# Kernel optimization log

Measured on AMD Instinct MI355X. Metric: run time of the kernel, lower is better.

The kernel has to match this reference:

```python
import jax, jax.numpy as jnp
import numpy as np

D_MODEL = 512
N_STATE = 64
EMB_DIM = 512
LN_EPS = 1e-5


def setup_inputs() -> dict:
    key = jax.random.key(0)
    ks = jax.random.split(key, 12)
    B, L, d, N, e = 8, 2048, D_MODEL, N_STATE, EMB_DIM
    x = jax.random.normal(ks[0], (B, L, d), dtype=jnp.float32)
    emb = jax.random.normal(ks[1], (B, e), dtype=jnp.float32)
    # S4D kernel params
    A_real = -0.5 * jnp.ones((d, N), dtype=jnp.float32)
    A_imag = jnp.pi * jnp.broadcast_to(jnp.arange(N, dtype=jnp.float32)[None, :], (d, N))
    C = jax.random.normal(ks[2], (d, N, 2), dtype=jnp.float32) * 0.5
    dt_min, dt_max = 0.001, 0.1
    log_dt = jax.random.uniform(ks[3], (d,), dtype=jnp.float32) * (np.log(dt_max) - np.log(dt_min)) + np.log(dt_min)
    B_ssm = jnp.ones((d, N), dtype=jnp.float32)  # buffer, treated as constant
    # block params
    D_skip = jax.random.normal(ks[4], (d,), dtype=jnp.float32) * 0.01
    ln_gamma = jnp.ones((d,), dtype=jnp.float32)
    ln_beta = jnp.zeros((d,), dtype=jnp.float32)
    lim_out = 1.0 / np.sqrt(d)
    W_out = jax.random.uniform(ks[5], (2 * d, d), dtype=jnp.float32, minval=-lim_out, maxval=lim_out)
    b_out = jax.random.uniform(ks[6], (2 * d,), dtype=jnp.float32, minval=-lim_out, maxval=lim_out)
    lim_f = 1.0 / np.sqrt(e)
    W_film = jax.random.uniform(ks[7], (2 * d, e), dtype=jnp.float32, minval=-lim_f, maxval=lim_f)
    b_film = jax.random.uniform(ks[8], (2 * d,), dtype=jnp.float32, minval=-lim_f, maxval=lim_f)
    return dict(x=x, emb=emb, A_real=A_real, A_imag=A_imag, C=C, log_dt=log_dt,
                B_ssm=B_ssm, D_skip=D_skip, ln_gamma=ln_gamma, ln_beta=ln_beta,
                W_out=W_out, b_out=b_out, W_film=W_film, b_film=b_film)


def reference(x, emb, A_real, A_imag, C, log_dt, B_ssm, D_skip, ln_gamma, ln_beta,
              W_out, b_out, W_film, b_film):
    Bsz, L, d = x.shape
    residual = x
    # LayerNorm
    mu = jnp.mean(x, axis=-1, keepdims=True)
    var = jnp.mean((x - mu) ** 2, axis=-1, keepdims=True)
    xn = (x - mu) * jax.lax.rsqrt(var + LN_EPS) * ln_gamma + ln_beta
    # S4D kernel: K[d,l] = Re( sum_n (C*B)[d,n] * exp(dt*A)[d,n]**l ) * dt[d]
    dt = jnp.exp(log_dt)                                 # (d,)
    A = A_real + 1j * A_imag                             # (d,N)
    dtA = A * dt[:, None]                                # (d,N)
    Cc = (C[..., 0] + 1j * C[..., 1]) * B_ssm            # (d,N) complex
    l = jnp.arange(L, dtype=jnp.float32)
    powers = jnp.exp(dtA[:, :, None] * l)                # (d,N,L) complex, A_bar**l
    K = jnp.einsum('dn,dnl->dl', Cc, powers).real * dt[:, None]  # (d,L)
    # FFT convolution (circular over 2L -> linear)
    x_t = jnp.transpose(xn, (0, 2, 1))                   # (B,d,L)
    K_f = jnp.fft.rfft(K, n=2 * L)                       # (d,L+1)
    x_f = jnp.fft.rfft(x_t, n=2 * L)                     # (B,d,L+1)
    y = jnp.fft.irfft(K_f[None] * x_f, n=2 * L)[..., :L] # (B,d,L)
    y = y + x_t * D_skip[None, :, None]
    y = jnp.transpose(y, (0, 2, 1))                      # (B,L,d)
    # FiLM conditioning
    film = jax.nn.silu(emb) @ W_film.T + b_film          # (B,2d)
    scale, shift = jnp.split(film, 2, axis=-1)
    y = y * (1.0 + scale[:, None, :]) + shift[:, None, :]
    # out_proj: Linear(d,2d) + GLU
    proj = y @ W_out.T + b_out                           # (B,L,2d)
    a, g = jnp.split(proj, 2, axis=-1)
    y = a * jax.nn.sigmoid(g)
    return residual + y
```

## Files before the change

kernel.cpp:

```cpp
#include <hip/hip_runtime.h>
#include <math.h>

typedef __attribute__((ext_vector_type(8))) short bf8v;
typedef __attribute__((ext_vector_type(4))) float f4v;

union BF8 { bf8v v; unsigned short e[8]; };

__device__ __forceinline__ float bf2f(unsigned short u) {
  union { unsigned int i; float f; } c; c.i = ((unsigned int)u) << 16; return c.f;
}
__device__ __forceinline__ unsigned short f2bf(float f) {
  union { float f; unsigned int i; } c; c.f = f;
  return (unsigned short)((c.i + 0x7fffu + ((c.i >> 16) & 1u)) >> 16);
}
__device__ __forceinline__ void gld16(const unsigned short* g, unsigned short* l) {
  __builtin_amdgcn_global_load_lds(
      (const __attribute__((address_space(1))) unsigned int*)g,
      (__attribute__((address_space(3))) unsigned int*)l, 16, 0, 0);
}

__global__ __launch_bounds__(64) void ln_kernel(const float* __restrict__ x,
    const float* __restrict__ gamma, const float* __restrict__ beta,
    unsigned short* __restrict__ xn) {
  const int row = blockIdx.x;
  const int lane = threadIdx.x;
  const float4* xr = (const float4*)(x + (size_t)row * 512);
  const float4 v0 = xr[lane * 2], v1 = xr[lane * 2 + 1];
  float s  = v0.x + v0.y + v0.z + v0.w + v1.x + v1.y + v1.z + v1.w;
  float sq = v0.x*v0.x + v0.y*v0.y + v0.z*v0.z + v0.w*v0.w
           + v1.x*v1.x + v1.y*v1.y + v1.z*v1.z + v1.w*v1.w;
  #pragma unroll
  for (int off = 32; off >= 1; off >>= 1) {
    s  += __shfl_xor(s, off);
    sq += __shfl_xor(sq, off);
  }
  const float mu   = s * (1.f / 512.f);
  const float var  = sq * (1.f / 512.f) - mu * mu;
  const float rstd = rsqrtf(var + 1e-5f);
  const float4* gp = (const float4*)gamma + lane * 2;
  const float4* bp = (const float4*)beta  + lane * 2;
  const float4 g0 = gp[0], g1 = gp[1], bb0 = bp[0], bb1 = bp[1];
  const float o0 = (v0.x - mu) * rstd * g0.x + bb0.x;
  const float o1 = (v0.y - mu) * rstd * g0.y + bb0.y;
  const float o2 = (v0.z - mu) * rstd * g0.z + bb0.z;
  const float o3 = (v0.w - mu) * rstd * g0.w + bb0.w;
  const float o4 = (v1.x - mu) * rstd * g1.x + bb1.x;
  const float o5 = (v1.y - mu) * rstd * g1.y + bb1.y;
  const float o6 = (v1.z - mu) * rstd * g1.z + bb1.z;
  const float o7 = (v1.w - mu) * rstd * g1.w + bb1.w;
  uint4 pk;
  pk.x = (unsigned)f2bf(o0) | ((unsigned)f2bf(o1) << 16);
  pk.y = (unsigned)f2bf(o2) | ((unsigned)f2bf(o3) << 16);
  pk.z = (unsigned)f2bf(o4) | ((unsigned)f2bf(o5) << 16);
  pk.w = (unsigned)f2bf(o6) | ((unsigned)f2bf(o7) << 16);
  ((uint4*)(xn + (size_t)row * 512))[lane] = pk;
}

__global__ __launch_bounds__(256) void film_kernel(const float* __restrict__ emb,
    const float* __restrict__ Wf, const float* __restrict__ bfm,
    float* __restrict__ film) {
  const int gw = blockIdx.x * 4 + (threadIdx.x >> 6);
  const int lane = threadIdx.x & 63;
  const int b = gw >> 10, j = gw & 1023;
  const float4* ep = (const float4*)(emb + (size_t)b * 512) + lane * 2;
  const float4* wp = (const float4*)(Wf + (size_t)j * 512) + lane * 2;
  float acc = 0.f;
  #pragma unroll
  for (int i = 0; i < 2; i++) {
    const float4 e = ep[i], w = wp[i];
    acc += (e.x / (1.f + __expf(-e.x))) * w.x;
    acc += (e.y / (1.f + __expf(-e.y))) * w.y;
    acc += (e.z / (1.f + __expf(-e.z))) * w.z;
    acc += (e.w / (1.f + __expf(-e.w))) * w.w;
  }
  #pragma unroll
  for (int off = 32; off >= 1; off >>= 1) acc += __shfl_xor(acc, off);
  if (lane == 0) film[(size_t)b * 1024 + j] = acc + bfm[j];
}

__global__ __launch_bounds__(256) void wcvt_kernel(const float* __restrict__ W,
    unsigned short* __restrict__ Wb) {
  const int i = blockIdx.x * 256 + threadIdx.x;
  const float4 v = ((const float4*)W)[i];
  uint2 pk;
  pk.x = (unsigned)f2bf(v.x) | ((unsigned)f2bf(v.y) << 16);
  pk.y = (unsigned)f2bf(v.z) | ((unsigned)f2bf(v.w) << 16);
  ((uint2*)Wb)[i] = pk;
}

__global__ __launch_bounds__(256) void tr_kernel(const unsigned short* __restrict__ in,
    unsigned short* __restrict__ out, int R, int C) {
  __shared__ __align__(16) unsigned short t[64 * 72];
  const int c0 = blockIdx.x * 64, r0 = blockIdx.y * 64;
  const int tid = threadIdx.x;
  #pragma unroll
  for (int i = 0; i < 2; i++) {
    const int idx = tid + i * 256;
    const int r = idx >> 3, q = idx & 7;
    const uint4 v = *(const uint4*)(in + (size_t)(r0 + r) * C + c0 + q * 8);
    *(uint4*)&t[r * 72 + ((q ^ (r >> 3)) * 8)] = v;
  }
  __syncthreads();
  #pragma unroll
  for (int i = 0; i < 2; i++) {
    const int idx = tid + i * 256;
    const int c = idx >> 3, g = idx & 7;
    union { unsigned short s[8]; uint4 u; } pk;
    #pragma unroll
    for (int j = 0; j < 8; j++)
      pk.s[j] = t[(g * 8 + j) * 72 + (((c >> 3) ^ g) * 8) + (c & 7)];
    *(uint4*)(out + (size_t)(c0 + c) * R + r0 + g * 8) = pk.u;
  }
}

__global__ __launch_bounds__(256) void ktab_kernel(const float* __restrict__ A_real,
    const float* __restrict__ A_imag, const float* __restrict__ Cc,
    const float* __restrict__ log_dt, const float* __restrict__ B_ssm,
    const float* __restrict__ D_skip, float* __restrict__ Kt) {
  const int d = blockIdx.x * 4 + (threadIdx.x >> 6);
  const int n = threadIdx.x & 63;
  const int dn = d * 64 + n;
  const float dt = __expf(log_dt[d]);
  const float er = __expf(dt * A_real[dn]);
  float sw, cw; __sincosf(dt * A_imag[dn], &sw, &cw);
  const float wre = er * cw, wim = er * sw;
  const float bs = B_ssm[dn] * dt;
  float pre = Cc[dn * 2] * bs, pim = Cc[dn * 2 + 1] * bs;
  const float dsk = D_skip[d];
  for (int tau = 0; tau < 64; tau++) {
    float r = pre;
    #pragma unroll
    for (int off = 32; off >= 1; off >>= 1) r += __shfl_xor(r, off);
    if (n == 0) Kt[d * 64 + tau] = (tau == 0) ? (r + dsk) : r;
    const float nre = pre * wre - pim * wim;
    const float nim = pre * wim + pim * wre;
    pre = nre; pim = nim;
  }
}

__global__ __launch_bounds__(256) void tab_kernel(
    const float* __restrict__ A_real, const float* __restrict__ A_imag,
    const float* __restrict__ Cc, const float* __restrict__ log_dt,
    const float* __restrict__ B_ssm, const float* __restrict__ Kt,
    unsigned short* __restrict__ Pre, unsigned short* __restrict__ Pim,
    unsigned short* __restrict__ Mre, unsigned short* __restrict__ Mim,
    unsigned short* __restrict__ Tt, float* __restrict__ W64r, float* __restrict__ W64i) {
  const int d = blockIdx.x;
  const int tid = threadIdx.x;
  const float dt = __expf(log_dt[d]);
  for (int g = tid; g < 512; g += 256) {
    const int n = g >> 3, s0 = (g & 7) * 8;
    const int dn = d * 64 + n;
    const float ar = dt * A_real[dn], ai = dt * A_imag[dn];
    union { unsigned short s[8]; uint4 u; } pr, pi;
    #pragma unroll
    for (int j = 0; j < 8; j++) {
      const float k = (float)(63 - (s0 + j));
      const float ex = __expf(ar * k);
      float sn, cs; __sincosf(ai * k, &sn, &cs);
      pr.s[j] = f2bf(ex * cs); pi.s[j] = f2bf(ex * sn);
    }
    *(uint4*)(Pre + (size_t)d * 4096 + n * 64 + s0) = pr.u;
    *(uint4*)(Pim + (size_t)d * 4096 + n * 64 + s0) = pi.u;
  }
  for (int g = tid; g < 512; g += 256) {
    const int t = g >> 3, n0 = (g & 7) * 8;
    union { unsigned short s[8]; uint4 u; } mr, mi;
    #pragma unroll
    for (int j = 0; j < 8; j++) {
      const int dn = d * 64 + n0 + j;
      const float ar = dt * A_real[dn], ai = dt * A_imag[dn];
      const float bs = B_ssm[dn] * dt;
      const float c0 = Cc[dn * 2] * bs, c1 = Cc[dn * 2 + 1] * bs;
      const float k = (float)(t + 1);
      const float ex = __expf(ar * k);
      float sn, cs; __sincosf(ai * k, &sn, &cs);
      mr.s[j] = f2bf(ex * (c0 * cs - c1 * sn));
      mi.s[j] = f2bf(-ex * (c0 * sn + c1 * cs));
    }
    *(uint4*)(Mre + (size_t)d * 4096 + t * 64 + n0) = mr.u;
    *(uint4*)(Mim + (size_t)d * 4096 + t * 64 + n0) = mi.u;
  }
  for (int g = tid; g < 512; g += 256) {
    const int t = g >> 3, s0 = (g & 7) * 8;
    union { unsigned short s[8]; uint4 u; } tv;
    #pragma unroll
    for (int j = 0; j < 8; j++) {
      const int s = s0 + j;
      tv.s[j] = (s <= t) ? f2bf(Kt[d * 64 + (t - s)]) : (unsigned short)0;
    }
    *(uint4*)(Tt + (size_t)d * 4096 + t * 64 + s0) = tv.u;
  }
  if (tid < 64) {
    const int dn = d * 64 + tid;
    const float ex = __expf(dt * A_real[dn] * 64.f);
    float sn, cs; __sincosf(dt * A_imag[dn] * 64.f, &sn, &cs);
    W64r[d * 64 + tid] = ex * cs;
    W64i[d * 64 + tid] = ex * sn;
  }
}

__global__ __launch_bounds__(256, 2) void ssm_kernel(
    const unsigned short* __restrict__ xT,
    const unsigned short* __restrict__ Pre, const unsigned short* __restrict__ Pim,
    const unsigned short* __restrict__ Mre, const unsigned short* __restrict__ Mim,
    const unsigned short* __restrict__ Tt,
    const float* __restrict__ W64r, const float* __restrict__ W64i,
    const float* __restrict__ film, unsigned short* __restrict__ y2) {
  extern __shared__ char smem[];
  unsigned int*   Eb  = (unsigned int*)smem;
  unsigned short* Ibr = (unsigned short*)(smem + 64 * 133 * 4);
  unsigned short* Ibi = Ibr + 128 * 72;

  const int bx = blockIdx.x;
  const int d = bx & 511, h = bx >> 9;
  const int tid = threadIdx.x;
  const int wv = tid >> 6, lane = tid & 63;
  const int n15 = lane & 15, quad = lane >> 4;
  const int j0 = wv * 32;
  const int jg0 = h * 128;
  const size_t dtab = (size_t)d * 4096;

  bf8v Xf[2][2];
  #pragma unroll
  for (int ct = 0; ct < 2; ct++)
    #pragma unroll
    for (int kq = 0; kq < 2; kq++) {
      const int j = j0 + ct * 16 + n15;
      Xf[ct][kq] = *(const bf8v*)(xT + (size_t)d * 16384 + (jg0 + j) * 64 + kq * 32 + quad * 8);
    }

  {
    f4v Er[4][2], Ei[4][2];
    #pragma unroll
    for (int a = 0; a < 4; a++)
      #pragma unroll
      for (int b2 = 0; b2 < 2; b2++) { Er[a][b2] = (f4v){0,0,0,0}; Ei[a][b2] = (f4v){0,0,0,0}; }
    #pragma unroll
    for (int mt = 0; mt < 4; mt++)
      #pragma unroll
      for (int kq = 0; kq < 2; kq++) {
        const bf8v pr = *(const bf8v*)(Pre + dtab + (mt * 16 + n15) * 64 + kq * 32 + quad * 8);
        const bf8v pi = *(const bf8v*)(Pim + dtab + (mt * 16 + n15) * 64 + kq * 32 + quad * 8);
        #pragma unroll
        for (int ct = 0; ct < 2; ct++) {
          Er[mt][ct] = __builtin_amdgcn_mfma_f32_16x16x32_bf16(pr, Xf[ct][kq], Er[mt][ct], 0, 0, 0);
          Ei[mt][ct] = __builtin_amdgcn_mfma_f32_16x16x32_bf16(pi, Xf[ct][kq], Ei[mt][ct], 0, 0, 0);
        }
      }
    #pragma unroll
    for (int mt = 0; mt < 4; mt++)
      #pragma unroll
      for (int ct = 0; ct < 2; ct++)
        #pragma unroll
        for (int i = 0; i < 4; i++) {
          const int row = mt * 16 + quad * 4 + i;
          const int col = j0 + ct * 16 + n15;
          Eb[row * 133 + col] =
              (unsigned)f2bf(Er[mt][ct][i]) | ((unsigned)f2bf(Ei[mt][ct][i]) << 16);
        }
  }
  __syncthreads();

  {
    const int n = tid & 63, bp = tid >> 6;
    const float wre = W64r[d * 64 + n], wim = W64i[d * 64 + n];
    unsigned int eb[32];
    #pragma unroll
    for (int c = 0; c < 32; c++) eb[c] = Eb[n * 133 + bp * 32 + c];
    float str = 0.f, sti = 0.f;
    #pragma unroll
    for (int c = 0; c < 32; c++) {
      const int j = bp * 32 + c;
      Ibr[j * 72 + n] = f2bf(str);
      Ibi[j * 72 + n] = f2bf(sti);
      const float er = bf2f((unsigned short)(eb[c] & 0xffffu));
      const float ei = bf2f((unsigned short)(eb[c] >> 16));
      const float nr = er + wre * str - wim * sti;
      const float ni = ei + wre * sti + wim * str;
      str = nr; sti = ni;
    }
  }
  __syncthreads();

  f4v Y[4][2];
  #pragma unroll
  for (int a = 0; a < 4; a++)
    #pragma unroll
    for (int b2 = 0; b2 < 2; b2++) Y[a][b2] = (f4v){0,0,0,0};

  #pragma unroll
  for (int mt = 0; mt < 4; mt++)
    #pragma unroll
    for (int kq = 0; kq < 2; kq++) {
      const bf8v tf = *(const bf8v*)(Tt + dtab + (mt * 16 + n15) * 64 + kq * 32 + quad * 8);
      #pragma unroll
      for (int ct = 0; ct < 2; ct++)
        Y[mt][ct] = __builtin_amdgcn_mfma_f32_16x16x32_bf16(tf, Xf[ct][kq], Y[mt][ct], 0, 0, 0);
    }

  #pragma unroll
  for (int kq = 0; kq < 2; kq++) {
    bf8v irf[2], iif[2];
    #pragma unroll
    for (int ct = 0; ct < 2; ct++) {
      const int j = j0 + ct * 16 + n15;
      irf[ct] = *(const bf8v*)&Ibr[j * 72 + kq * 32 + quad * 8];
      iif[ct] = *(const bf8v*)&Ibi[j * 72 + kq * 32 + quad * 8];
    }
    #pragma unroll
    for (int mt = 0; mt < 4; mt++) {
      const bf8v mr = *(const bf8v*)(Mre + dtab + (mt * 16 + n15) * 64 + kq * 32 + quad * 8);
      const bf8v mi = *(const bf8v*)(Mim + dtab + (mt * 16 + n15) * 64 + kq * 32 + quad * 8);
      #pragma unroll
      for (int ct = 0; ct < 2; ct++) {
        Y[mt][ct] = __builtin_amdgcn_mfma_f32_16x16x32_bf16(mr, irf[ct], Y[mt][ct], 0, 0, 0);
        Y[mt][ct] = __builtin_amdgcn_mfma_f32_16x16x32_bf16(mi, iif[ct], Y[mt][ct], 0, 0, 0);
      }
    }
  }

  #pragma unroll
  for (int ct = 0; ct < 2; ct++) {
    const int jl = j0 + ct * 16 + n15;
    const int jglob = jg0 + jl;
    const int b = jglob >> 5;
    const float scl = 1.f + film[b * 1024 + d];
    const float shf = film[b * 1024 + 512 + d];
    #pragma unroll
    for (int mt = 0; mt < 4; mt++) {
      union { unsigned short s[4]; uint2 u; } pk;
      #pragma unroll
      for (int i = 0; i < 4; i++)
        pk.s[i] = f2bf(fmaf(Y[mt][ct][i], scl, shf));
      *(uint2*)(y2 + (size_t)d * 16384 + jglob * 64 + mt * 16 + quad * 4) = pk.u;
    }
  }
}

__global__ __launch_bounds__(256, 3) void gemm_kernel(
    const unsigned short* __restrict__ y2n, const unsigned short* __restrict__ Wb,
    const float* __restrict__ bo, const float* __restrict__ x,
    float* __restrict__ out) {
  __shared__ __align__(16) unsigned short Al[128 * 32];
  __shared__ __align__(16) unsigned short Bl[128 * 32];
  const int m0 = blockIdx.x * 128, ct = blockIdx.y;
  const int tid = threadIdx.x;
  const int wv = tid >> 6, lane = tid & 63;
  const int n15 = lane & 15, quad = lane >> 4;
  const int srow = lane >> 2;
  const int sk = (lane & 3) * 8;

  f4v acc[2][8];
  #pragma unroll
  for (int mi = 0; mi < 2; mi++)
    #pragma unroll
    for (int t4 = 0; t4 < 8; t4++) acc[mi][t4] = (f4v){0.f, 0.f, 0.f, 0.f};

  for (int kk = 0; kk < 16; kk++) {
    #pragma unroll
    for (int i = 0; i < 2; i++) {
      const int row = wv * 32 + i * 16 + srow;
      gld16(y2n + (size_t)(m0 + row) * 512 + kk * 32 + sk, Al + wv * 1024 + i * 512);
      const int c = (row < 64) ? (ct * 64 + row) : (512 + ct * 64 + (row - 64));
      gld16(Wb + (size_t)c * 512 + kk * 32 + sk, Bl + wv * 1024 + i * 512);
    }
    __syncthreads();
    bf8v a0 = *(const bf8v*)&Al[(wv * 32 + n15) * 32 + quad * 8];
    bf8v a1 = *(const bf8v*)&Al[(wv * 32 + 16 + n15) * 32 + quad * 8];
    #pragma unroll
    for (int t4 = 0; t4 < 8; t4++) {
      const bf8v bb = *(const bf8v*)&Bl[(t4 * 16 + n15) * 32 + quad * 8];
      acc[0][t4] = __builtin_amdgcn_mfma_f32_16x16x32_bf16(a0, bb, acc[0][t4], 0, 0, 0);
      acc[1][t4] = __builtin_amdgcn_mfma_f32_16x16x32_bf16(a1, bb, acc[1][t4], 0, 0, 0);
    }
    __syncthreads();
  }
  #pragma unroll
  for (int mi = 0; mi < 2; mi++) {
    const int mrow = m0 + wv * 32 + mi * 16 + quad * 4;
    #pragma unroll
    for (int t4 = 0; t4 < 4; t4++) {
      const int c = ct * 64 + t4 * 16 + n15;
      const float ba = bo[c], bg = bo[512 + c];
      #pragma unroll
      for (int i = 0; i < 4; i++) {
        const size_t off = (size_t)(mrow + i) * 512 + c;
        const float av = acc[mi][t4][i] + ba;
        const float gv = acc[mi][t4 + 4][i] + bg;
        out[off] = x[off] + av * (1.f / (1.f + __expf(-gv)));
      }
    }
  }
}

extern "C" void kernel_launch(void* const* d_in, const int* in_sizes, int n_in,
                              void* d_out, int out_size, void* d_ws, size_t ws_size,
                              hipStream_t stream) {
  const float* x      = (const float*)d_in[0];
  const float* emb    = (const float*)d_in[1];
  const float* A_real = (const float*)d_in[2];
  const float* A_imag = (const float*)d_in[3];
  const float* C      = (const float*)d_in[4];
  const float* log_dt = (const float*)d_in[5];
  const float* B_ssm  = (const float*)d_in[6];
  const float* D_skip = (const float*)d_in[7];
  const float* gamma  = (const float*)d_in[8];
  const float* beta   = (const float*)d_in[9];
  const float* W_out  = (const float*)d_in[10];
  const float* b_out  = (const float*)d_in[11];
  const float* W_film = (const float*)d_in[12];
  const float* b_film = (const float*)d_in[13];
  float* out = (float*)d_out;

  char* ws = (char*)d_ws;
  size_t o = 0;
  float*          film = (float*)(ws + o);          o += 32768;
  unsigned short* xn   = (unsigned short*)(ws + o); o += 16777216;
  unsigned short* xT   = (unsigned short*)(ws + o); o += 16777216;
  float*          Kt   = (float*)(ws + o);          o += 131072;
  unsigned short* Wb   = (unsigned short*)(ws + o); o += 1048576;
  unsigned short* Pre  = (unsigned short*)(ws + o); o += 4194304;
  unsigned short* Pim  = (unsigned short*)(ws + o); o += 4194304;
  unsigned short* Mre  = (unsigned short*)(ws + o); o += 4194304;
  unsigned short* Mim  = (unsigned short*)(ws + o); o += 4194304;
  unsigned short* Tt   = (unsigned short*)(ws + o); o += 4194304;
  float*          W64r = (float*)(ws + o);          o += 131072;
  float*          W64i = (float*)(ws + o);          o += 131072;
  unsigned short* y2   = xn;
  unsigned short* y2n  = xT;

  film_kernel<<<dim3(2048), dim3(256), 0, stream>>>(emb, W_film, b_film, film);
  ln_kernel<<<dim3(16384), dim3(64), 0, stream>>>(x, gamma, beta, xn);
  wcvt_kernel<<<dim3(512), dim3(256), 0, stream>>>(W_out, Wb);
  ktab_kernel<<<dim3(128), dim3(256), 0, stream>>>(A_real, A_imag, C, log_dt, B_ssm, D_skip, Kt);
  tab_kernel<<<dim3(512), dim3(256), 0, stream>>>(A_real, A_imag, C, log_dt, B_ssm, Kt,
                                                  Pre, Pim, Mre, Mim, Tt, W64r, W64i);
  tr_kernel<<<dim3(8, 256), dim3(256), 0, stream>>>(xn, xT, 16384, 512);
  ssm_kernel<<<dim3(1024), dim3(256), 70912, stream>>>(xT, Pre, Pim, Mre, Mim, Tt,
                                                       W64r, W64i, film, y2);
  tr_kernel<<<dim3(256, 8), dim3(256), 0, stream>>>(y2, y2n, 512, 16384);
  gemm_kernel<<<dim3(128, 8), dim3(256), 0, stream>>>(y2n, Wb, b_out, x, out);
}
```

Baseline: 205.3 us.

## Fuse prelude kernels, fuse LayerNorm with transpose, shrink SSM tiles, widen GEMM K-step

Film, weight conversion, kernel-tap and table generation are merged into one prelude launch, and the K taps are now computed directly in shared memory instead of through a global buffer. LayerNorm now writes its transposed output directly, which removes one transpose pass and the intermediate buffer. The SSM kernel uses half-size blocks with static shared memory and targets higher occupancy. The GEMM uses a 64-wide K step with XOR-swizzled LDS. The gain comes from fewer launches and less memory traffic, at the cost of more blocks and a different load balance.

```diff
diff --git a/kernel.cpp b/kernel.cpp
--- a/kernel.cpp
+++ b/kernel.cpp
@@ -19,73 +19,173 @@
       (__attribute__((address_space(3))) unsigned int*)l, 16, 0, 0);
 }
 
-__global__ __launch_bounds__(64) void ln_kernel(const float* __restrict__ x,
+__global__ __launch_bounds__(256) void prelude_kernel(
+    const float* __restrict__ emb, const float* __restrict__ Wf,
+    const float* __restrict__ bfm, float* __restrict__ film,
+    const float* __restrict__ W, unsigned short* __restrict__ Wb,
+    const float* __restrict__ A_real, const float* __restrict__ A_imag,
+    const float* __restrict__ Cc, const float* __restrict__ log_dt,
+    const float* __restrict__ B_ssm, const float* __restrict__ D_skip,
+    unsigned short* __restrict__ Pre, unsigned short* __restrict__ Pim,
+    unsigned short* __restrict__ Mre, unsigned short* __restrict__ Mim,
+    unsigned short* __restrict__ Tt, float* __restrict__ W64r, float* __restrict__ W64i) {
+  __shared__ float Ktl[64];
+  const int blk = blockIdx.x;
+  const int tid = threadIdx.x;
+  if (blk < 2048) {
+    const int gw = blk * 4 + (tid >> 6);
+    const int lane = tid & 63;
+    const int b = gw >> 10, j = gw & 1023;
+    const float4* ep = (const float4*)(emb + (size_t)b * 512) + lane * 2;
+    const float4* wp = (const float4*)(Wf + (size_t)j * 512) + lane * 2;
+    float acc = 0.f;
+    #pragma unroll
+    for (int i = 0; i < 2; i++) {
+      const float4 e = ep[i], w = wp[i];
+      acc += (e.x / (1.f + __expf(-e.x))) * w.x;
+      acc += (e.y / (1.f + __expf(-e.y))) * w.y;
+      acc += (e.z / (1.f + __expf(-e.z))) * w.z;
+      acc += (e.w / (1.f + __expf(-e.w))) * w.w;
+    }
+    #pragma unroll
+    for (int off = 32; off >= 1; off >>= 1) acc += __shfl_xor(acc, off);
+    if (lane == 0) film[(size_t)b * 1024 + j] = acc + bfm[j];
+  } else if (blk < 2560) {
+    const int i = (blk - 2048) * 256 + tid;
+    const float4 v = ((const float4*)W)[i];
+    uint2 pk;
+    pk.x = (unsigned)f2bf(v.x) | ((unsigned)f2bf(v.y) << 16);
+    pk.y = (unsigned)f2bf(v.z) | ((unsigned)f2bf(v.w) << 16);
+    ((uint2*)Wb)[i] = pk;
+  } else {
+    const int d = blk - 2560;
+    const float dt = __expf(log_dt[d]);
+    const int wv = tid >> 6, n = tid & 63;
+    {
+      const int dn = d * 64 + n;
+      const float ar = dt * A_real[dn], ai = dt * A_imag[dn];
+      const float bs = B_ssm[dn] * dt;
+      const float c0 = Cc[dn * 2] * bs, c1 = Cc[dn * 2 + 1] * bs;
+      #pragma unroll
+      for (int i = 0; i < 16; i++) {
+        const float tau = (float)(wv * 16 + i);
+        const float ex = __expf(ar * tau);
+        float sn, cs; __sincosf(ai * tau, &sn, &cs);
+        float r = ex * (c0 * cs - c1 * sn);
+        #pragma unroll
+        for (int off = 32; off >= 1; off >>= 1) r += __shfl_xor(r, off);
+        if (n == 0) Ktl[wv * 16 + i] = (wv * 16 + i == 0) ? (r + D_skip[d]) : r;
+      }
+    }
+    __syncthreads();
+    for (int g = tid; g < 512; g += 256) {
+      const int nn = g >> 3, s0 = (g & 7) * 8;
+      const int dn = d * 64 + nn;
+      const float ar = dt * A_real[dn], ai = dt * A_imag[dn];
+      union { unsigned short s[8]; uint4 u; } pr, pi;
+      #pragma unroll
+      for (int j = 0; j < 8; j++) {
+        const float k = (float)(63 - (s0 + j));
+        const float ex = __expf(ar * k);
+        float sn, cs; __sincosf(ai * k, &sn, &cs);
+        pr.s[j] = f2bf(ex * cs); pi.s[j] = f2bf(ex * sn);
+      }
+      *(uint4*)(Pre + (size_t)d * 4096 + nn * 64 + s0) = pr.u;
+      *(uint4*)(Pim + (size_t)d * 4096 + nn * 64 + s0) = pi.u;
+    }
+    for (int g = tid; g < 512; g += 256) {
+      const int t = g >> 3, n0 = (g & 7) * 8;
+      union { unsigned short s[8]; uint4 u; } mr, mi;
+      #pragma unroll
+      for (int j = 0; j < 8; j++) {
+        const int dn = d * 64 + n0 + j;
+        const float ar = dt * A_real[dn], ai = dt * A_imag[dn];
+        const float bs = B_ssm[dn] * dt;
+        const float c0 = Cc[dn * 2] * bs, c1 = Cc[dn * 2 + 1] * bs;
+        const float k = (float)(t + 1);
+        const float ex = __expf(ar * k);
+        float sn, cs; __sincosf(ai * k, &sn, &cs);
+        mr.s[j] = f2bf(ex * (c0 * cs - c1 * sn));
+        mi.s[j] = f2bf(-ex * (c0 * sn + c1 * cs));
+      }
+      *(uint4*)(Mre + (size_t)d * 4096 + t * 64 + n0) = mr.u;
+      *(uint4*)(Mim + (size_t)d * 4096 + t * 64 + n0) = mi.u;
+    }
+    for (int g = tid; g < 512; g += 256) {
+      const int t = g >> 3, s0 = (g & 7) * 8;
+      union { unsigned short s[8]; uint4 u; } tv;
+      #pragma unroll
+      for (int j = 0; j < 8; j++) {
+        const int s = s0 + j;
+        tv.s[j] = (s <= t) ? f2bf(Ktl[t - s]) : (unsigned short)0;
+      }
+      *(uint4*)(Tt + (size_t)d * 4096 + t * 64 + s0) = tv.u;
+    }
+    if (tid < 64) {
+      const int dn = d * 64 + tid;
+      const float ex = __expf(dt * A_real[dn] * 64.f);
+      float sn, cs; __sincosf(dt * A_imag[dn] * 64.f, &sn, &cs);
+      W64r[d * 64 + tid] = ex * cs;
+      W64i[d * 64 + tid] = ex * sn;
+    }
+  }
+}
+
+__global__ __launch_bounds__(256) void lnt_kernel(const float* __restrict__ x,
     const float* __restrict__ gamma, const float* __restrict__ beta,
-    unsigned short* __restrict__ xn) {
-  const int row = blockIdx.x;
-  const int lane = threadIdx.x;
-  const float4* xr = (const float4*)(x + (size_t)row * 512);
-  const float4 v0 = xr[lane * 2], v1 = xr[lane * 2 + 1];
-  float s  = v0.x + v0.y + v0.z + v0.w + v1.x + v1.y + v1.z + v1.w;
-  float sq = v0.x*v0.x + v0.y*v0.y + v0.z*v0.z + v0.w*v0.w
-           + v1.x*v1.x + v1.y*v1.y + v1.z*v1.z + v1.w*v1.w;
-  #pragma unroll
-  for (int off = 32; off >= 1; off >>= 1) {
-    s  += __shfl_xor(s, off);
-    sq += __shfl_xor(sq, off);
-  }
-  const float mu   = s * (1.f / 512.f);
-  const float var  = sq * (1.f / 512.f) - mu * mu;
-  const float rstd = rsqrtf(var + 1e-5f);
+    unsigned short* __restrict__ xT) {
+  __shared__ __align__(16) unsigned short t[16 * 520];
+  const int r0 = blockIdx.x * 16;
+  const int tid = threadIdx.x, wv = tid >> 6, lane = tid & 63;
   const float4* gp = (const float4*)gamma + lane * 2;
   const float4* bp = (const float4*)beta  + lane * 2;
   const float4 g0 = gp[0], g1 = gp[1], bb0 = bp[0], bb1 = bp[1];
-  const float o0 = (v0.x - mu) * rstd * g0.x + bb0.x;
-  const float o1 = (v0.y - mu) * rstd * g0.y + bb0.y;
-  const float o2 = (v0.z - mu) * rstd * g0.z + bb0.z;
-  const float o3 = (v0.w - mu) * rstd * g0.w + bb0.w;
-  const float o4 = (v1.x - mu) * rstd * g1.x + bb1.x;
-  const float o5 = (v1.y - mu) * rstd * g1.y + bb1.y;
-  const float o6 = (v1.z - mu) * rstd * g1.z + bb1.z;
-  const float o7 = (v1.w - mu) * rstd * g1.w + bb1.w;
-  uint4 pk;
-  pk.x = (unsigned)f2bf(o0) | ((unsigned)f2bf(o1) << 16);
-  pk.y = (unsigned)f2bf(o2) | ((unsigned)f2bf(o3) << 16);
-  pk.z = (unsigned)f2bf(o4) | ((unsigned)f2bf(o5) << 16);
-  pk.w = (unsigned)f2bf(o6) | ((unsigned)f2bf(o7) << 16);
-  ((uint4*)(xn + (size_t)row * 512))[lane] = pk;
-}
-
-__global__ __launch_bounds__(256) void film_kernel(const float* __restrict__ emb,
-    const float* __restrict__ Wf, const float* __restrict__ bfm,
-    float* __restrict__ film) {
-  const int gw = blockIdx.x * 4 + (threadIdx.x >> 6);
-  const int lane = threadIdx.x & 63;
-  const int b = gw >> 10, j = gw & 1023;
-  const float4* ep = (const float4*)(emb + (size_t)b * 512) + lane * 2;
-  const float4* wp = (const float4*)(Wf + (size_t)j * 512) + lane * 2;
-  float acc = 0.f;
-  #pragma unroll
-  for (int i = 0; i < 2; i++) {
-    const float4 e = ep[i], w = wp[i];
-    acc += (e.x / (1.f + __expf(-e.x))) * w.x;
-    acc += (e.y / (1.f + __expf(-e.y))) * w.y;
-    acc += (e.z / (1.f + __expf(-e.z))) * w.z;
-    acc += (e.w / (1.f + __expf(-e.w))) * w.w;
-  }
-  #pragma unroll
-  for (int off = 32; off >= 1; off >>= 1) acc += __shfl_xor(acc, off);
-  if (lane == 0) film[(size_t)b * 1024 + j] = acc + bfm[j];
-}
-
-__global__ __launch_bounds__(256) void wcvt_kernel(const float* __restrict__ W,
-    unsigned short* __restrict__ Wb) {
-  const int i = blockIdx.x * 256 + threadIdx.x;
-  const float4 v = ((const float4*)W)[i];
-  uint2 pk;
-  pk.x = (unsigned)f2bf(v.x) | ((unsigned)f2bf(v.y) << 16);
-  pk.y = (unsigned)f2bf(v.z) | ((unsigned)f2bf(v.w) << 16);
-  ((uint2*)Wb)[i] = pk;
+  #pragma unroll
+  for (int i = 0; i < 4; i++) {
+    const int r = wv * 4 + i;
+    const float4* xr = (const float4*)(x + (size_t)(r0 + r) * 512) + lane * 2;
+    const float4 v0 = xr[0], v1 = xr[1];
+    float s  = v0.x + v0.y + v0.z + v0.w + v1.x + v1.y + v1.z + v1.w;
+    float sq = v0.x*v0.x + v0.y*v0.y + v0.z*v0.z + v0.w*v0.w
+             + v1.x*v1.x + v1.y*v1.y + v1.z*v1.z + v1.w*v1.w;
+    #pragma unroll
+    for (int off = 32; off >= 1; off >>= 1) {
+      s  += __shfl_xor(s, off);
+      sq += __shfl_xor(sq, off);
+    }
+    const float mu   = s * (1.f / 512.f);
+    const float var  = sq * (1.f / 512.f) - mu * mu;
+    const float rstd = rsqrtf(var + 1e-5f);
+    uint4 pk;
+    pk.x = (unsigned)f2bf((v0.x - mu) * rstd * g0.x + bb0.x)
+         | ((unsigned)f2bf((v0.y - mu) * rstd * g0.y + bb0.y) << 16);
+    pk.y = (unsigned)f2bf((v0.z - mu) * rstd * g0.z + bb0.z)
+         | ((unsigned)f2bf((v0.w - mu) * rstd * g0.w + bb0.w) << 16);
+    pk.z = (unsigned)f2bf((v1.x - mu) * rstd * g1.x + bb1.x)
+         | ((unsigned)f2bf((v1.y - mu) * rstd * g1.y + bb1.y) << 16);
+    pk.w = (unsigned)f2bf((v1.z - mu) * rstd * g1.z + bb1.z)
+         | ((unsigned)f2bf((v1.w - mu) * rstd * g1.w + bb1.w) << 16);
+    *(uint4*)&t[r * 520 + lane * 8] = pk;
+  }
+  __syncthreads();
+  const int p = tid;
+  union { unsigned short s[8]; uint4 u; } a0, a1, b0, b1;
+  #pragma unroll
+  for (int r = 0; r < 8; r++) {
+    const unsigned v = *(const unsigned*)&t[r * 520 + p * 2];
+    a0.s[r] = (unsigned short)(v & 0xffffu);
+    b0.s[r] = (unsigned short)(v >> 16);
+  }
+  #pragma unroll
+  for (int r = 0; r < 8; r++) {
+    const unsigned v = *(const unsigned*)&t[(r + 8) * 520 + p * 2];
+    a1.s[r] = (unsigned short)(v & 0xffffu);
+    b1.s[r] = (unsigned short)(v >> 16);
+  }
+  unsigned short* o0 = xT + (size_t)(2 * p) * 16384 + r0;
+  *(uint4*)o0 = a0.u; *(uint4*)(o0 + 8) = a1.u;
+  unsigned short* o1 = xT + (size_t)(2 * p + 1) * 16384 + r0;
+  *(uint4*)o1 = b0.u; *(uint4*)(o1 + 8) = b1.u;
 }
 
 __global__ __launch_bounds__(256) void tr_kernel(const unsigned short* __restrict__ in,
@@ -113,217 +213,104 @@
   }
 }
 
-__global__ __launch_bounds__(256) void ktab_kernel(const float* __restrict__ A_real,
-    const float* __restrict__ A_imag, const float* __restrict__ Cc,
-    const float* __restrict__ log_dt, const float* __restrict__ B_ssm,
-    const float* __restrict__ D_skip, float* __restrict__ Kt) {
-  const int d = blockIdx.x * 4 + (threadIdx.x >> 6);
-  const int n = threadIdx.x & 63;
-  const int dn = d * 64 + n;
-  const float dt = __expf(log_dt[d]);
-  const float er = __expf(dt * A_real[dn]);
-  float sw, cw; __sincosf(dt * A_imag[dn], &sw, &cw);
-  const float wre = er * cw, wim = er * sw;
-  const float bs = B_ssm[dn] * dt;
-  float pre = Cc[dn * 2] * bs, pim = Cc[dn * 2 + 1] * bs;
-  const float dsk = D_skip[d];
-  for (int tau = 0; tau < 64; tau++) {
-    float r = pre;
-    #pragma unroll
-    for (int off = 32; off >= 1; off >>= 1) r += __shfl_xor(r, off);
-    if (n == 0) Kt[d * 64 + tau] = (tau == 0) ? (r + dsk) : r;
-    const float nre = pre * wre - pim * wim;
-    const float nim = pre * wim + pim * wre;
-    pre = nre; pim = nim;
-  }
-}
-
-__global__ __launch_bounds__(256) void tab_kernel(
-    const float* __restrict__ A_real, const float* __restrict__ A_imag,
-    const float* __restrict__ Cc, const float* __restrict__ log_dt,
-    const float* __restrict__ B_ssm, const float* __restrict__ Kt,
-    unsigned short* __restrict__ Pre, unsigned short* __restrict__ Pim,
-    unsigned short* __restrict__ Mre, unsigned short* __restrict__ Mim,
-    unsigned short* __restrict__ Tt, float* __restrict__ W64r, float* __restrict__ W64i) {
-  const int d = blockIdx.x;
-  const int tid = threadIdx.x;
-  const float dt = __expf(log_dt[d]);
-  for (int g = tid; g < 512; g += 256) {
-    const int n = g >> 3, s0 = (g & 7) * 8;
-    const int dn = d * 64 + n;
-    const float ar = dt * A_real[dn], ai = dt * A_imag[dn];
-    union { unsigned short s[8]; uint4 u; } pr, pi;
-    #pragma unroll
-    for (int j = 0; j < 8; j++) {
-      const float k = (float)(63 - (s0 + j));
-      const float ex = __expf(ar * k);
-      float sn, cs; __sincosf(ai * k, &sn, &cs);
-      pr.s[j] = f2bf(ex * cs); pi.s[j] = f2bf(ex * sn);
-    }
-    *(uint4*)(Pre + (size_t)d * 4096 + n * 64 + s0) = pr.u;
-    *(uint4*)(Pim + (size_t)d * 4096 + n * 64 + s0) = pi.u;
-  }
-  for (int g = tid; g < 512; g += 256) {
-    const int t = g >> 3, n0 = (g & 7) * 8;
-    union { unsigned short s[8]; uint4 u; } mr, mi;
-    #pragma unroll
-    for (int j = 0; j < 8; j++) {
-      const int dn = d * 64 + n0 + j;
-      const float ar = dt * A_real[dn], ai = dt * A_imag[dn];
-      const float bs = B_ssm[dn] * dt;
-      const float c0 = Cc[dn * 2] * bs, c1 = Cc[dn * 2 + 1] * bs;
-      const float k = (float)(t + 1);
-      const float ex = __expf(ar * k);
-      float sn, cs; __sincosf(ai * k, &sn, &cs);
-      mr.s[j] = f2bf(ex * (c0 * cs - c1 * sn));
-      mi.s[j] = f2bf(-ex * (c0 * sn + c1 * cs));
-    }
-    *(uint4*)(Mre + (size_t)d * 4096 + t * 64 + n0) = mr.u;
-    *(uint4*)(Mim + (size_t)d * 4096 + t * 64 + n0) = mi.u;
-  }
-  for (int g = tid; g < 512; g += 256) {
-    const int t = g >> 3, s0 = (g & 7) * 8;
-    union { unsigned short s[8]; uint4 u; } tv;
-    #pragma unroll
-    for (int j = 0; j < 8; j++) {
-      const int s = s0 + j;
-      tv.s[j] = (s <= t) ? f2bf(Kt[d * 64 + (t - s)]) : (unsigned short)0;
-    }
-    *(uint4*)(Tt + (size_t)d * 4096 + t * 64 + s0) = tv.u;
-  }
-  if (tid < 64) {
-    const int dn = d * 64 + tid;
-    const float ex = __expf(dt * A_real[dn] * 64.f);
-    float sn, cs; __sincosf(dt * A_imag[dn] * 64.f, &sn, &cs);
-    W64r[d * 64 + tid] = ex * cs;
-    W64i[d * 64 + tid] = ex * sn;
-  }
-}
-
-__global__ __launch_bounds__(256, 2) void ssm_kernel(
+__global__ __launch_bounds__(256, 4) void ssm_kernel(
     const unsigned short* __restrict__ xT,
     const unsigned short* __restrict__ Pre, const unsigned short* __restrict__ Pim,
     const unsigned short* __restrict__ Mre, const unsigned short* __restrict__ Mim,
     const unsigned short* __restrict__ Tt,
     const float* __restrict__ W64r, const float* __restrict__ W64i,
     const float* __restrict__ film, unsigned short* __restrict__ y2) {
-  extern __shared__ char smem[];
-  unsigned int*   Eb  = (unsigned int*)smem;
-  unsigned short* Ibr = (unsigned short*)(smem + 64 * 133 * 4);
-  unsigned short* Ibi = Ibr + 128 * 72;
+  __shared__ unsigned int Eb[64 * 66];
+  __shared__ unsigned short Ibr[64 * 72], Ibi[64 * 72];
 
   const int bx = blockIdx.x;
   const int d = bx & 511, h = bx >> 9;
   const int tid = threadIdx.x;
   const int wv = tid >> 6, lane = tid & 63;
   const int n15 = lane & 15, quad = lane >> 4;
-  const int j0 = wv * 32;
-  const int jg0 = h * 128;
+  const int j0 = wv * 16;
+  const int jg0 = h * 64;
   const size_t dtab = (size_t)d * 4096;
 
-  bf8v Xf[2][2];
-  #pragma unroll
-  for (int ct = 0; ct < 2; ct++)
-    #pragma unroll
-    for (int kq = 0; kq < 2; kq++) {
-      const int j = j0 + ct * 16 + n15;
-      Xf[ct][kq] = *(const bf8v*)(xT + (size_t)d * 16384 + (jg0 + j) * 64 + kq * 32 + quad * 8);
-    }
+  bf8v Xf[2];
+  #pragma unroll
+  for (int kq = 0; kq < 2; kq++)
+    Xf[kq] = *(const bf8v*)(xT + (size_t)d * 16384 + (jg0 + j0 + n15) * 64 + kq * 32 + quad * 8);
 
   {
-    f4v Er[4][2], Ei[4][2];
-    #pragma unroll
-    for (int a = 0; a < 4; a++)
-      #pragma unroll
-      for (int b2 = 0; b2 < 2; b2++) { Er[a][b2] = (f4v){0,0,0,0}; Ei[a][b2] = (f4v){0,0,0,0}; }
+    f4v Er[4], Ei[4];
+    #pragma unroll
+    for (int a = 0; a < 4; a++) { Er[a] = (f4v){0,0,0,0}; Ei[a] = (f4v){0,0,0,0}; }
     #pragma unroll
     for (int mt = 0; mt < 4; mt++)
       #pragma unroll
       for (int kq = 0; kq < 2; kq++) {
         const bf8v pr = *(const bf8v*)(Pre + dtab + (mt * 16 + n15) * 64 + kq * 32 + quad * 8);
         const bf8v pi = *(const bf8v*)(Pim + dtab + (mt * 16 + n15) * 64 + kq * 32 + quad * 8);
-        #pragma unroll
-        for (int ct = 0; ct < 2; ct++) {
-          Er[mt][ct] = __builtin_amdgcn_mfma_f32_16x16x32_bf16(pr, Xf[ct][kq], Er[mt][ct], 0, 0, 0);
-          Ei[mt][ct] = __builtin_amdgcn_mfma_f32_16x16x32_bf16(pi, Xf[ct][kq], Ei[mt][ct], 0, 0, 0);
-        }
+        Er[mt] = __builtin_amdgcn_mfma_f32_16x16x32_bf16(pr, Xf[kq], Er[mt], 0, 0, 0);
+        Ei[mt] = __builtin_amdgcn_mfma_f32_16x16x32_bf16(pi, Xf[kq], Ei[mt], 0, 0, 0);
       }
     #pragma unroll
     for (int mt = 0; mt < 4; mt++)
       #pragma unroll
-      for (int ct = 0; ct < 2; ct++)
-        #pragma unroll
-        for (int i = 0; i < 4; i++) {
-          const int row = mt * 16 + quad * 4 + i;
-          const int col = j0 + ct * 16 + n15;
-          Eb[row * 133 + col] =
-              (unsigned)f2bf(Er[mt][ct][i]) | ((unsigned)f2bf(Ei[mt][ct][i]) << 16);
-        }
+      for (int i = 0; i < 4; i++) {
+        const int row = mt * 16 + quad * 4 + i;
+        Eb[row * 66 + j0 + n15] =
+            (unsigned)f2bf(Er[mt][i]) | ((unsigned)f2bf(Ei[mt][i]) << 16);
+      }
   }
   __syncthreads();
 
   {
     const int n = tid & 63, bp = tid >> 6;
-    const float wre = W64r[d * 64 + n], wim = W64i[d * 64 + n];
-    unsigned int eb[32];
-    #pragma unroll
-    for (int c = 0; c < 32; c++) eb[c] = Eb[n * 133 + bp * 32 + c];
-    float str = 0.f, sti = 0.f;
-    #pragma unroll
-    for (int c = 0; c < 32; c++) {
-      const int j = bp * 32 + c;
-      Ibr[j * 72 + n] = f2bf(str);
-      Ibi[j * 72 + n] = f2bf(sti);
-      const float er = bf2f((unsigned short)(eb[c] & 0xffffu));
-      const float ei = bf2f((unsigned short)(eb[c] >> 16));
-      const float nr = er + wre * str - wim * sti;
-      const float ni = ei + wre * sti + wim * str;
-      str = nr; sti = ni;
+    if (bp < 2) {
+      const float wre = W64r[d * 64 + n], wim = W64i[d * 64 + n];
+      unsigned int eb[32];
+      #pragma unroll
+      for (int c = 0; c < 32; c++) eb[c] = Eb[n * 66 + bp * 32 + c];
+      float str = 0.f, sti = 0.f;
+      #pragma unroll
+      for (int c = 0; c < 32; c++) {
+        const int j = bp * 32 + c;
+        Ibr[j * 72 + n] = f2bf(str);
+        Ibi[j * 72 + n] = f2bf(sti);
+        const float er = bf2f((unsigned short)(eb[c] & 0xffffu));
+        const float ei = bf2f((unsigned short)(eb[c] >> 16));
+        const float nr = er + wre * str - wim * sti;
+        const float ni = ei + wre * sti + wim * str;
+        str = nr; sti = ni;
+      }
     }
   }
   __syncthreads();
 
-  f4v Y[4][2];
-  #pragma unroll
-  for (int a = 0; a < 4; a++)
-    #pragma unroll
-    for (int b2 = 0; b2 < 2; b2++) Y[a][b2] = (f4v){0,0,0,0};
+  f4v Y[4];
+  #pragma unroll
+  for (int a = 0; a < 4; a++) Y[a] = (f4v){0,0,0,0};
 
   #pragma unroll
   for (int mt = 0; mt < 4; mt++)
     #pragma unroll
     for (int kq = 0; kq < 2; kq++) {
       const bf8v tf = *(const bf8v*)(Tt + dtab + (mt * 16 + n15) * 64 + kq * 32 + quad * 8);
-      #pragma unroll
-      for (int ct = 0; ct < 2; ct++)
-        Y[mt][ct] = __builtin_amdgcn_mfma_f32_16x16x32_bf16(tf, Xf[ct][kq], Y[mt][ct], 0, 0, 0);
+      Y[mt] = __builtin_amdgcn_mfma_f32_16x16x32_bf16(tf, Xf[kq], Y[mt], 0, 0, 0);
     }
 
   #pragma unroll
   for (int kq = 0; kq < 2; kq++) {
-    bf8v irf[2], iif[2];
-    #pragma unroll
-    for (int ct = 0; ct < 2; ct++) {
-      const int j = j0 + ct * 16 + n15;
-      irf[ct] = *(const bf8v*)&Ibr[j * 72 + kq * 32 + quad * 8];
-      iif[ct] = *(const bf8v*)&Ibi[j * 72 + kq * 32 + quad * 8];
-    }
+    const bf8v irf = *(const bf8v*)&Ibr[(j0 + n15) * 72 + kq * 32 + quad * 8];
+    const bf8v iif = *(const bf8v*)&Ibi[(j0 + n15) * 72 + kq * 32 + quad * 8];
     #pragma unroll
     for (int mt = 0; mt < 4; mt++) {
       const bf8v mr = *(const bf8v*)(Mre + dtab + (mt * 16 + n15) * 64 + kq * 32 + quad * 8);
       const bf8v mi = *(const bf8v*)(Mim + dtab + (mt * 16 + n15) * 64 + kq * 32 + quad * 8);
-      #pragma unroll
-      for (int ct = 0; ct < 2; ct++) {
-        Y[mt][ct] = __builtin_amdgcn_mfma_f32_16x16x32_bf16(mr, irf[ct], Y[mt][ct], 0, 0, 0);
-        Y[mt][ct] = __builtin_amdgcn_mfma_f32_16x16x32_bf16(mi, iif[ct], Y[mt][ct], 0, 0, 0);
-      }
-    }
-  }
-
-  #pragma unroll
-  for (int ct = 0; ct < 2; ct++) {
-    const int jl = j0 + ct * 16 + n15;
-    const int jglob = jg0 + jl;
+      Y[mt] = __builtin_amdgcn_mfma_f32_16x16x32_bf16(mr, irf, Y[mt], 0, 0, 0);
+      Y[mt] = __builtin_amdgcn_mfma_f32_16x16x32_bf16(mi, iif, Y[mt], 0, 0, 0);
+    }
+  }
+
+  {
+    const int jglob = jg0 + j0 + n15;
     const int b = jglob >> 5;
     const float scl = 1.f + film[b * 1024 + d];
     const float shf = film[b * 1024 + 512 + d];
@@ -332,7 +319,7 @@
       union { unsigned short s[4]; uint2 u; } pk;
       #pragma unroll
       for (int i = 0; i < 4; i++)
-        pk.s[i] = f2bf(fmaf(Y[mt][ct][i], scl, shf));
+        pk.s[i] = f2bf(fmaf(Y[mt][i], scl, shf));
       *(uint2*)(y2 + (size_t)d * 16384 + jglob * 64 + mt * 16 + quad * 4) = pk.u;
     }
   }
@@ -342,14 +329,14 @@
     const unsigned short* __restrict__ y2n, const unsigned short* __restrict__ Wb,
     const float* __restrict__ bo, const float* __restrict__ x,
     float* __restrict__ out) {
-  __shared__ __align__(16) unsigned short Al[128 * 32];
-  __shared__ __align__(16) unsigned short Bl[128 * 32];
+  __shared__ __align__(16) unsigned short Al[128 * 64];
+  __shared__ __align__(16) unsigned short Bl[128 * 64];
   const int m0 = blockIdx.x * 128, ct = blockIdx.y;
   const int tid = threadIdx.x;
   const int wv = tid >> 6, lane = tid & 63;
   const int n15 = lane & 15, quad = lane >> 4;
-  const int srow = lane >> 2;
-  const int sk = (lane & 3) * 8;
+  const int sr = lane >> 3;
+  const int sk = ((lane & 7) ^ sr) * 8;
 
   f4v acc[2][8];
   #pragma unroll
@@ -357,22 +344,28 @@
     #pragma unroll
     for (int t4 = 0; t4 < 8; t4++) acc[mi][t4] = (f4v){0.f, 0.f, 0.f, 0.f};
 
-  for (int kk = 0; kk < 16; kk++) {
-    #pragma unroll
-    for (int i = 0; i < 2; i++) {
-      const int row = wv * 32 + i * 16 + srow;
-      gld16(y2n + (size_t)(m0 + row) * 512 + kk * 32 + sk, Al + wv * 1024 + i * 512);
-      const int c = (row < 64) ? (ct * 64 + row) : (512 + ct * 64 + (row - 64));
-      gld16(Wb + (size_t)c * 512 + kk * 32 + sk, Bl + wv * 1024 + i * 512);
+  for (int kk = 0; kk < 8; kk++) {
+    #pragma unroll
+    for (int c = 0; c < 4; c++) {
+      const int row = wv * 32 + c * 8 + sr;
+      gld16(y2n + (size_t)(m0 + row) * 512 + kk * 64 + sk, Al + wv * 2048 + c * 512);
+      const int cg = (row < 64) ? (ct * 64 + row) : (512 + ct * 64 + (row - 64));
+      gld16(Wb + (size_t)cg * 512 + kk * 64 + sk, Bl + wv * 2048 + c * 512);
     }
     __syncthreads();
-    bf8v a0 = *(const bf8v*)&Al[(wv * 32 + n15) * 32 + quad * 8];
-    bf8v a1 = *(const bf8v*)&Al[(wv * 32 + 16 + n15) * 32 + quad * 8];
-    #pragma unroll
-    for (int t4 = 0; t4 < 8; t4++) {
-      const bf8v bb = *(const bf8v*)&Bl[(t4 * 16 + n15) * 32 + quad * 8];
-      acc[0][t4] = __builtin_amdgcn_mfma_f32_16x16x32_bf16(a0, bb, acc[0][t4], 0, 0, 0);
-      acc[1][t4] = __builtin_amdgcn_mfma_f32_16x16x32_bf16(a1, bb, acc[1][t4], 0, 0, 0);
+    #pragma unroll
+    for (int kq = 0; kq < 2; kq++) {
+      const int r0 = wv * 32 + n15;
+      const int r1 = r0 + 16;
+      const bf8v a0 = *(const bf8v*)&Al[r0 * 64 + (((kq * 4 + quad) ^ (r0 & 7)) * 8)];
+      const bf8v a1 = *(const bf8v*)&Al[r1 * 64 + (((kq * 4 + quad) ^ (r1 & 7)) * 8)];
+      #pragma unroll
+      for (int t4 = 0; t4 < 8; t4++) {
+        const int rb = t4 * 16 + n15;
+        const bf8v bb = *(const bf8v*)&Bl[rb * 64 + (((kq * 4 + quad) ^ (rb & 7)) * 8)];
+        acc[0][t4] = __builtin_amdgcn_mfma_f32_16x16x32_bf16(a0, bb, acc[0][t4], 0, 0, 0);
+        acc[1][t4] = __builtin_amdgcn_mfma_f32_16x16x32_bf16(a1, bb, acc[1][t4], 0, 0, 0);
+      }
     }
     __syncthreads();
   }
@@ -416,9 +409,7 @@
   char* ws = (char*)d_ws;
   size_t o = 0;
   float*          film = (float*)(ws + o);          o += 32768;
-  unsigned short* xn   = (unsigned short*)(ws + o); o += 16777216;
   unsigned short* xT   = (unsigned short*)(ws + o); o += 16777216;
-  float*          Kt   = (float*)(ws + o);          o += 131072;
   unsigned short* Wb   = (unsigned short*)(ws + o); o += 1048576;
   unsigned short* Pre  = (unsigned short*)(ws + o); o += 4194304;
   unsigned short* Pim  = (unsigned short*)(ws + o); o += 4194304;
@@ -427,18 +418,16 @@
   unsigned short* Tt   = (unsigned short*)(ws + o); o += 4194304;
   float*          W64r = (float*)(ws + o);          o += 131072;
   float*          W64i = (float*)(ws + o);          o += 131072;
-  unsigned short* y2   = xn;
-  unsigned short* y2n  = xT;
-
-  film_kernel<<<dim3(2048), dim3(256), 0, stream>>>(emb, W_film, b_film, film);
-  ln_kernel<<<dim3(16384), dim3(64), 0, stream>>>(x, gamma, beta, xn);
-  wcvt_kernel<<<dim3(512), dim3(256), 0, stream>>>(W_out, Wb);
-  ktab_kernel<<<dim3(128), dim3(256), 0, stream>>>(A_real, A_imag, C, log_dt, B_ssm, D_skip, Kt);
-  tab_kernel<<<dim3(512), dim3(256), 0, stream>>>(A_real, A_imag, C, log_dt, B_ssm, Kt,
-                                                  Pre, Pim, Mre, Mim, Tt, W64r, W64i);
-  tr_kernel<<<dim3(8, 256), dim3(256), 0, stream>>>(xn, xT, 16384, 512);
-  ssm_kernel<<<dim3(1024), dim3(256), 70912, stream>>>(xT, Pre, Pim, Mre, Mim, Tt,
-                                                       W64r, W64i, film, y2);
+  unsigned short* y2   = (unsigned short*)(ws + o); o += 16777216;
+  unsigned short* y2n  = (unsigned short*)(ws + o); o += 16777216;
+
+  prelude_kernel<<<dim3(3072), dim3(256), 0, stream>>>(
+      emb, W_film, b_film, film, W_out, Wb,
+      A_real, A_imag, C, log_dt, B_ssm, D_skip,
+      Pre, Pim, Mre, Mim, Tt, W64r, W64i);
+  lnt_kernel<<<dim3(1024), dim3(256), 0, stream>>>(x, gamma, beta, xT);
+  ssm_kernel<<<dim3(2048), dim3(256), 0, stream>>>(xT, Pre, Pim, Mre, Mim, Tt,
+                                                   W64r, W64i, film, y2);
   tr_kernel<<<dim3(256, 8), dim3(256), 0, stream>>>(y2, y2n, 512, 16384);
   gemm_kernel<<<dim3(128, 8), dim3(256), 0, stream>>>(y2n, Wb, b_out, x, out);
 }
```

New measurement: 196.4 us. 1.05x faster.
